# Kernel optimization log

Hardware: AMD Instinct MI355X
Metric: run time of the kernel (lower is better)

The kernel has to match this reference:

```python
import jax, jax.numpy as jnp
import numpy as np
import math

EPS = 1e-6          # eps for safe cumprod / clamping
CHUNK = 4           # chunk_size w
SHARP = 1.0         # sharpening_factor
NOISE_STD = 1.0
N_HEADS = 4
ADIM = 512


def moving_sum(x, back, forward):
    """Windowed running sum over last axis: out[k] = sum_{j=k-back}^{k+forward} x[j].
    Equivalent to the conv1d trick in the original (all-ones filter)."""
    k = x.shape[-1]
    pad = [(0, 0)] * (x.ndim - 1) + [(back, forward)]
    c = jnp.cumsum(jnp.pad(x, pad), axis=-1)
    c0 = jnp.concatenate([jnp.zeros_like(c[..., :1]), c], axis=-1)
    w = back + forward
    return c0[..., w + 1: w + 1 + k] - c0[..., :k]


def setup_inputs() -> dict:
    rng = jax.random.key(0)
    ks = jax.random.split(rng, 12)
    B, qlen, klen, kdim, qdim, adim = 8, 256, 2048, 512, 512, ADIM
    s = 0.02
    return {
        "key_enc": jax.random.normal(ks[0], (B, klen, kdim), jnp.float32),
        "query":   jax.random.normal(ks[1], (B, qlen, qdim), jnp.float32),
        "noise":   jax.random.normal(ks[2], (B, qlen, klen), jnp.float32),
        # monotonic energy params
        "Wk_m": jax.random.normal(ks[3], (kdim, adim), jnp.float32) * s,
        "bk_m": jnp.zeros((adim,), jnp.float32),
        "Wq_m": jax.random.normal(ks[4], (qdim, adim), jnp.float32) * s,
        "bq_m": jnp.zeros((adim,), jnp.float32),
        "r":    jnp.array([-4.0], jnp.float32),
        # chunkwise energy params (multi-head)
        "Wk_c": jax.random.normal(ks[5], (kdim, adim), jnp.float32) * s,
        "bk_c": jnp.zeros((adim,), jnp.float32),
        "Wq_c": jax.random.normal(ks[6], (qdim, adim), jnp.float32) * s,
        "bq_c": jnp.zeros((adim,), jnp.float32),
    }


def _mocha_beta(key_enc, query, noise, Wk_m, bk_m, Wq_m, bq_m, r,
                Wk_c, bk_c, Wq_c, bq_c):
    B, klen, _ = key_enc.shape
    qlen = query.shape[1]
    H = N_HEADS
    dk = ADIM // H
    scale = math.sqrt(ADIM)

    # --- monotonic energy (single head): [B, qlen, klen]
    k_m = key_enc @ Wk_m + bk_m
    q_m = query @ Wq_m + bq_m
    e_mono = jnp.einsum('bqa,bka->bqk', q_m, k_m) / scale + r[0]

    # --- p_choose with additive gaussian noise (encourages discreteness)
    p_choose = jax.nn.sigmoid(e_mono + noise * NOISE_STD)  # [B,q,k]

    # --- safe cumprod of (1 - p) via exclusive cumsum in log space
    log1mp = jnp.log(jnp.clip(1.0 - p_choose, EPS, 1.0))
    cumprod_1mp = jnp.exp(jnp.cumsum(log1mp, axis=-1) - log1mp)  # exclusive

    # --- monotonic alpha recurrence over query steps (parallel-mode MoChA)
    aw0 = jnp.zeros((B, klen), jnp.float32).at[:, 0].set(1.0)

    def step(aw_prev, inp):
        p_i, cp_i = inp  # [B, klen]
        alpha_i = p_i * cp_i * jnp.cumsum(
            aw_prev / jnp.clip(cp_i, EPS, 1.0), axis=-1)
        return alpha_i, alpha_i

    xs = (jnp.swapaxes(p_choose, 0, 1), jnp.swapaxes(cumprod_1mp, 0, 1))
    _, alpha_q = jax.lax.scan(step, aw0, xs)          # [q, B, k]
    alpha = jnp.swapaxes(alpha_q, 0, 1)                # [B, q, k]

    # --- chunkwise energy (multi-head): [B, H, q, k]
    k_c = (key_enc @ Wk_c + bk_c).reshape(B, klen, H, dk)
    q_c = (query @ Wq_c + bq_c).reshape(B, qlen, H, dk)
    e_chunk = jnp.einsum('bqhd,bkhd->bhqk', q_c, k_c) / scale

    # --- efficient chunkwise attention (clipped-logit moving-sum softmax)
    e = e_chunk - jnp.max(e_chunk, axis=3, keepdims=True)
    softmax_exp = jnp.maximum(jnp.exp(e), 1e-5)
    denom = moving_sum(softmax_exp, back=CHUNK - 1, forward=0)
    beta = softmax_exp * moving_sum(
        alpha[:, None] * SHARP / denom, back=0, forward=CHUNK - 1)
    return beta  # [B, H, q, k]


def reference(key_enc, query, noise, Wk_m, bk_m, Wq_m, bq_m, r,
              Wk_c, bk_c, Wq_c, bq_c):
    return _mocha_beta(key_enc, query, noise, Wk_m, bk_m, Wq_m, bq_m, r,
                       Wk_c, bk_c, Wq_c, bq_c)
```

## Files before the change

### kernel.cpp

```cpp
#include <hip/hip_runtime.h>
#include <math.h>

#define BATCH   8
#define QLEN    256
#define KLEN    2048
#define KDIM    512
#define ADIMC   512
#define NHEADS  4
#define DKH     128
#define CHUNKW  4

static constexpr float INV_SCALE = 0.04419417382415922f;
static constexpr float EPSV = 1e-6f;

typedef __attribute__((ext_vector_type(8))) short bf16x8;
typedef __attribute__((ext_vector_type(4))) float f32x4;

__device__ __forceinline__ unsigned short f2bf(float f) {
    unsigned u = __builtin_bit_cast(unsigned, f);
    u += 0x7fffu + ((u >> 16) & 1u);
    return (unsigned short)(u >> 16);
}

__device__ __forceinline__ void lds_barrier() {
    __asm__ volatile("s_waitcnt lgkmcnt(0)\n\ts_barrier" ::: "memory");
}

__device__ __forceinline__ void gload_lds16(const void* g, void* l) {
    __builtin_amdgcn_global_load_lds(
        (const __attribute__((address_space(1))) void*)g,
        (__attribute__((address_space(3))) void*)l, 16, 0, 0);
}

__global__ __launch_bounds__(256) void cast_bf16(
    const float* __restrict__ x, unsigned short* __restrict__ y, int n4)
{
    int i = blockIdx.x * 256 + threadIdx.x;
    if (i < n4) {
        float4 v = ((const float4*)x)[i];
        ushort4 o;
        o.x = f2bf(v.x); o.y = f2bf(v.y); o.z = f2bf(v.z); o.w = f2bf(v.w);
        ((ushort4*)y)[i] = o;
    }
}

__global__ __launch_bounds__(256) void transpose_cast(
    const float* __restrict__ W, unsigned short* __restrict__ WT)
{
    __shared__ float tile[32][33];
    const int tx = threadIdx.x;
    const int ty = threadIdx.y;
    const int k0 = blockIdx.y * 32, n0 = blockIdx.x * 32;
    #pragma unroll
    for (int i = 0; i < 32; i += 8)
        tile[ty + i][tx] = W[(size_t)(k0 + ty + i) * KDIM + n0 + tx];
    __syncthreads();
    #pragma unroll
    for (int i = 0; i < 32; i += 8)
        WT[(size_t)(n0 + ty + i) * KDIM + k0 + tx] = f2bf(tile[tx][ty + i]);
}

template<int KSTEPS>
__device__ __forceinline__ void mfma_nt_staged(
    const unsigned short* __restrict__ A, const unsigned short* __restrict__ B,
    int lda, int ldb, int bm, int bn,
    unsigned short* AsLDS, unsigned short* BsLDS, f32x4 acc[4][4])
{
    const int t = threadIdx.x;
    const int wv = t >> 6, ln = t & 63;
    const int r = ln & 15, quad = ln >> 4;
    const int wm = (wv >> 1) * 64, wn = (wv & 1) * 64;
    const int srow = wv * 16 + (ln >> 2);
    const int scol = (ln & 3) * 8;

    for (int ks = 0; ks < KSTEPS; ++ks) {
        const int k0 = ks * 32;
        #pragma unroll
        for (int j = 0; j < 2; ++j) {
            gload_lds16(A + (size_t)(bm + j * 64 + srow) * lda + k0 + scol,
                        AsLDS + (size_t)(j * 64 + wv * 16) * 32);
            gload_lds16(B + (size_t)(bn + j * 64 + srow) * ldb + k0 + scol,
                        BsLDS + (size_t)(j * 64 + wv * 16) * 32);
        }
        __syncthreads();
        bf16x8 af[4], bg[4];
        #pragma unroll
        for (int f = 0; f < 4; ++f)
            af[f] = *(const bf16x8*)(AsLDS + (size_t)(wm + f * 16 + r) * 32 + quad * 8);
        #pragma unroll
        for (int f = 0; f < 4; ++f)
            bg[f] = *(const bf16x8*)(BsLDS + (size_t)(wn + f * 16 + r) * 32 + quad * 8);
        #pragma unroll
        for (int i = 0; i < 4; ++i)
            #pragma unroll
            for (int j2 = 0; j2 < 4; ++j2)
                acc[i][j2] = __builtin_amdgcn_mfma_f32_16x16x32_bf16(
                    af[i], bg[j2], acc[i][j2], 0, 0, 0);
        __syncthreads();
    }
}

__device__ __forceinline__ void zero_acc(f32x4 acc[4][4]) {
    #pragma unroll
    for (int i = 0; i < 4; ++i)
        #pragma unroll
        for (int j = 0; j < 4; ++j)
            acc[i][j] = f32x4{0.f, 0.f, 0.f, 0.f};
}

__global__ __launch_bounds__(256) void proj_mfma(
    const unsigned short* __restrict__ A, const unsigned short* __restrict__ WT,
    const float* __restrict__ bias_m, const float* __restrict__ bias_c,
    unsigned short* __restrict__ C)
{
    __shared__ unsigned short As[128 * 32];
    __shared__ unsigned short Bs[128 * 32];
    const int bm = blockIdx.y * 128, bn = blockIdx.x * 128;
    f32x4 acc[4][4]; zero_acc(acc);
    mfma_nt_staged<16>(A, WT, KDIM, KDIM, bm, bn, As, Bs, acc);
    const int wv = threadIdx.x >> 6, ln = threadIdx.x & 63;
    const int r = ln & 15, quad = ln >> 4;
    const int m0 = bm + (wv >> 1) * 64, n0 = bn + (wv & 1) * 64;
    #pragma unroll
    for (int j = 0; j < 4; ++j) {
        const int n = n0 + j * 16 + r;
        const float bv = (n < 512) ? bias_m[n] : bias_c[n - 512];
        #pragma unroll
        for (int i = 0; i < 4; ++i) {
            #pragma unroll
            for (int reg = 0; reg < 4; ++reg) {
                const int m = m0 + i * 16 + quad * 4 + reg;
                C[(size_t)m * 1024 + n] = f2bf(acc[i][j][reg] + bv);
            }
        }
    }
}

__global__ __launch_bounds__(256) void pchoose_mfma(
    const unsigned short* __restrict__ qp, const unsigned short* __restrict__ kp,
    const float* __restrict__ noise, const float* __restrict__ rp,
    float* __restrict__ p)
{
    __shared__ unsigned short As[128 * 32];
    __shared__ unsigned short Bs[128 * 32];
    const int b = blockIdx.z;
    const unsigned short* A = qp + (size_t)b * QLEN * 1024;
    const unsigned short* B = kp + (size_t)b * KLEN * 1024;
    const int bm = blockIdx.y * 128, bn = blockIdx.x * 128;
    f32x4 acc[4][4]; zero_acc(acc);
    mfma_nt_staged<16>(A, B, 1024, 1024, bm, bn, As, Bs, acc);
    const int wv = threadIdx.x >> 6, ln = threadIdx.x & 63;
    const int r = ln & 15, quad = ln >> 4;
    const int m0 = bm + (wv >> 1) * 64, n0 = bn + (wv & 1) * 64;
    const float rv = rp[0];
    #pragma unroll
    for (int i = 0; i < 4; ++i) {
        #pragma unroll
        for (int reg = 0; reg < 4; ++reg) {
            const int q = m0 + i * 16 + quad * 4 + reg;
            const size_t rowoff = ((size_t)b * QLEN + q) * KLEN;
            #pragma unroll
            for (int j = 0; j < 4; ++j) {
                const int k = n0 + j * 16 + r;
                const float e = acc[i][j][reg] * INV_SCALE + rv + noise[rowoff + k];
                p[rowoff + k] = __builtin_amdgcn_rcpf(1.0f + __expf(-e));
            }
        }
    }
}

__global__ __launch_bounds__(256) void echunk_mfma(
    const unsigned short* __restrict__ qp, const unsigned short* __restrict__ kp,
    float* __restrict__ out)
{
    __shared__ unsigned short As[128 * 32];
    __shared__ unsigned short Bs[128 * 32];
    const int z = blockIdx.z, b = z >> 2, h = z & 3;
    const unsigned short* A = qp + (size_t)b * QLEN * 1024 + 512 + h * DKH;
    const unsigned short* B = kp + (size_t)b * KLEN * 1024 + 512 + h * DKH;
    const int bm = blockIdx.y * 128, bn = blockIdx.x * 128;
    f32x4 acc[4][4]; zero_acc(acc);
    mfma_nt_staged<4>(A, B, 1024, 1024, bm, bn, As, Bs, acc);
    const int wv = threadIdx.x >> 6, ln = threadIdx.x & 63;
    const int r = ln & 15, quad = ln >> 4;
    const int m0 = bm + (wv >> 1) * 64, n0 = bn + (wv & 1) * 64;
    #pragma unroll
    for (int i = 0; i < 4; ++i) {
        #pragma unroll
        for (int reg = 0; reg < 4; ++reg) {
            const int q = m0 + i * 16 + quad * 4 + reg;
            const size_t rowoff = (((size_t)z) * QLEN + q) * KLEN;
            #pragma unroll
            for (int j = 0; j < 4; ++j) {
                const int k = n0 + j * 16 + r;
                out[rowoff + k] = acc[i][j][reg] * INV_SCALE;
            }
        }
    }
}

__device__ __forceinline__ float wave_incl_scan(float x)
{
#define DPP_ADD(ctrl, rmask, bctrl)                                            \
    { int _t = __builtin_amdgcn_update_dpp(0, __builtin_bit_cast(int, x),      \
                                           ctrl, rmask, 0xf, bctrl);           \
      x += __builtin_bit_cast(float, _t); }
    DPP_ADD(0x111, 0xf, true)
    DPP_ADD(0x112, 0xf, true)
    DPP_ADD(0x114, 0xf, true)
    DPP_ADD(0x118, 0xf, true)
    DPP_ADD(0x142, 0xa, false)
    DPP_ADD(0x143, 0xc, false)
#undef DPP_ADD
    return x;
}

__global__ __launch_bounds__(256) void cumprod_mr(
    const float* __restrict__ p, float* __restrict__ mArr, float* __restrict__ rArr)
{
    const size_t row = blockIdx.x;
    const float* pr = p + row * KLEN;
    float* mr = mArr + row * KLEN;
    float* rr = rArr + row * KLEN;
    const int tid = threadIdx.x;
    const int lane = tid & 63, wid = tid >> 6;
    __shared__ float waveTot[4];

    float4 v0 = *(const float4*)(pr + tid * 8);
    float4 v1 = *(const float4*)(pr + tid * 8 + 4);
    float pv[8] = {v0.x, v0.y, v0.z, v0.w, v1.x, v1.y, v1.z, v1.w};
    float excl[8];
    float run = 0.0f;
    #pragma unroll
    for (int j = 0; j < 8; ++j) {
        float l = __logf(fminf(fmaxf(1.0f - pv[j], EPSV), 1.0f));
        excl[j] = run;
        run += l;
    }
    float s = wave_incl_scan(run);
    if (lane == 63) waveTot[wid] = s;
    __syncthreads();
    float wex = 0.0f;
    for (int w = 0; w < wid; ++w) wex += waveTot[w];
    const float texcl = wex + s - run;

    float mv[8], rv[8];
    #pragma unroll
    for (int j = 0; j < 8; ++j) {
        const float cpv = __expf(texcl + excl[j]);
        mv[j] = pv[j] * cpv;
        rv[j] = __builtin_amdgcn_rcpf(fminf(fmaxf(cpv, EPSV), 1.0f));
    }
    *(float4*)(mr + tid * 8)     = *(float4*)&mv[0];
    *(float4*)(mr + tid * 8 + 4) = *(float4*)&mv[4];
    *(float4*)(rr + tid * 8)     = *(float4*)&rv[0];
    *(float4*)(rr + tid * 8 + 4) = *(float4*)&rv[4];
}

__global__ __launch_bounds__(512, 1) void alpha_scan(
    const float* __restrict__ mArr, const float* __restrict__ rArr,
    float* __restrict__ alpha)
{
    const int b = blockIdx.x;
    const int tid = threadIdx.x;
    const int lane = tid & 63, wid = tid >> 6;
    __shared__ __align__(16) float wt[2][8];

    const float* mrow = mArr + (size_t)b * QLEN * KLEN + tid * 4;
    const float* rrow = rArr + (size_t)b * QLEN * KLEN + tid * 4;
    float* arow = alpha + (size_t)b * QLEN * KLEN + tid * 4;

    float aw0 = 0.f, aw1 = 0.f, aw2 = 0.f, aw3 = 0.f;
    if (tid == 0) aw0 = 1.0f;

    float4 mA = *(const float4*)(mrow);
    float4 rA = *(const float4*)(rrow);
    float4 mB = *(const float4*)(mrow + KLEN);
    float4 rB = *(const float4*)(rrow + KLEN);

#define ASTEP(I, MREG, RREG)                                                   \
    {                                                                          \
        const int i_ = (I);                                                    \
        float4 mc = MREG, rc = RREG;                                           \
        const int rn_ = (i_ + 2 < QLEN) ? (i_ + 2) : (QLEN - 1);               \
        MREG = *(const float4*)(mrow + (size_t)rn_ * KLEN);                    \
        RREG = *(const float4*)(rrow + (size_t)rn_ * KLEN);                    \
        float run = 0.0f, i0, i1, i2, i3;                                      \
        run = fmaf(aw0, rc.x, run); i0 = run;                                  \
        run = fmaf(aw1, rc.y, run); i1 = run;                                  \
        run = fmaf(aw2, rc.z, run); i2 = run;                                  \
        run = fmaf(aw3, rc.w, run); i3 = run;                                  \
        float tot = wave_incl_scan(run);                                       \
        if (lane == 63) wt[i_ & 1][wid] = tot;                                 \
        lds_barrier();                                                         \
        float base = tot - run;                                                \
        float4 w0 = *(const float4*)&wt[i_ & 1][0];                            \
        float4 w1 = *(const float4*)&wt[i_ & 1][4];                            \
        if (wid > 0) base += w0.x;                                             \
        if (wid > 1) base += w0.y;                                             \
        if (wid > 2) base += w0.z;                                             \
        if (wid > 3) base += w0.w;                                             \
        if (wid > 4) base += w1.x;                                             \
        if (wid > 5) base += w1.y;                                             \
        if (wid > 6) base += w1.z;                                             \
        aw0 = mc.x * (base + i0);                                              \
        aw1 = mc.y * (base + i1);                                              \
        aw2 = mc.z * (base + i2);                                              \
        aw3 = mc.w * (base + i3);                                              \
        float4 ov; ov.x = aw0; ov.y = aw1; ov.z = aw2; ov.w = aw3;             \
        *(float4*)(arow + (size_t)i_ * KLEN) = ov;                             \
    }

    for (int io = 0; io < QLEN; io += 2) {
        ASTEP(io + 0, mA, rA)
        ASTEP(io + 1, mB, rB)
    }
#undef ASTEP
}

__global__ __launch_bounds__(256) void beta_kernel(
    float* __restrict__ eo, const float* __restrict__ alpha)
{
    __shared__ float sse[KLEN + 3];
    __shared__ float su[KLEN + 3];
    __shared__ float wmax[4];

    const int tid = threadIdx.x;
    const int lane = tid & 63, wid = tid >> 6;
    const int row = blockIdx.x;
    const int q = row & (QLEN - 1);
    const int b = row >> 10;
    float* erow = eo + (size_t)row * KLEN;
    const float* arow = alpha + ((size_t)b * QLEN + q) * KLEN;

    if (tid < 3) { sse[tid] = 0.0f; su[KLEN + tid] = 0.0f; }

    float ev[8];
    float lm = -INFINITY;
    #pragma unroll
    for (int j = 0; j < 8; ++j) {
        const int k = tid + 256 * j;
        ev[j] = erow[k];
        lm = fmaxf(lm, ev[j]);
    }
    #pragma unroll
    for (int off = 32; off > 0; off >>= 1) lm = fmaxf(lm, __shfl_xor(lm, off));
    if (lane == 0) wmax[wid] = lm;
    __syncthreads();
    const float mx = fmaxf(fmaxf(wmax[0], wmax[1]), fmaxf(wmax[2], wmax[3]));

    #pragma unroll
    for (int j = 0; j < 8; ++j) {
        const int k = tid + 256 * j;
        sse[k + 3] = fmaxf(__expf(ev[j] - mx), 1e-5f);
    }
    __syncthreads();

    #pragma unroll
    for (int j = 0; j < 8; ++j) {
        const int k = tid + 256 * j;
        const float denom = sse[k + 3] + sse[k + 2] + sse[k + 1] + sse[k];
        su[k] = arow[k] * __builtin_amdgcn_rcpf(denom);
    }
    __syncthreads();

    #pragma unroll
    for (int j = 0; j < 8; ++j) {
        const int k = tid + 256 * j;
        erow[k] = sse[k + 3] * (su[k] + su[k + 1] + su[k + 2] + su[k + 3]);
    }
}

extern "C" void kernel_launch(void* const* d_in, const int* in_sizes, int n_in,
                              void* d_out, int out_size, void* d_ws, size_t ws_size,
                              hipStream_t stream)
{
    (void)in_sizes; (void)n_in; (void)out_size; (void)ws_size;
    const float* key_enc = (const float*)d_in[0];
    const float* query   = (const float*)d_in[1];
    const float* noise   = (const float*)d_in[2];
    const float* Wk_m    = (const float*)d_in[3];
    const float* bk_m    = (const float*)d_in[4];
    const float* Wq_m    = (const float*)d_in[5];
    const float* bq_m    = (const float*)d_in[6];
    const float* rp      = (const float*)d_in[7];
    const float* Wk_c    = (const float*)d_in[8];
    const float* bk_c    = (const float*)d_in[9];
    const float* Wq_c    = (const float*)d_in[10];
    const float* bq_c    = (const float*)d_in[11];
    float* out = (float*)d_out;

    char* w = (char*)d_ws;
    unsigned short* kx    = (unsigned short*)w; w += (size_t)BATCH * KLEN * KDIM * 2;
    unsigned short* qx    = (unsigned short*)w; w += (size_t)BATCH * QLEN * KDIM * 2;
    unsigned short* WTk   = (unsigned short*)w; w += (size_t)1024 * KDIM * 2;
    unsigned short* WTq   = (unsigned short*)w; w += (size_t)1024 * KDIM * 2;
    unsigned short* kproj = (unsigned short*)w; w += (size_t)BATCH * KLEN * 1024 * 2;
    unsigned short* qproj = (unsigned short*)w; w += (size_t)BATCH * QLEN * 1024 * 2;
    float* p_alpha = (float*)w; w += (size_t)BATCH * QLEN * KLEN * 4;
    float* mArr    = (float*)w; w += (size_t)BATCH * QLEN * KLEN * 4;
    float* rArr    = (float*)w;

    hipLaunchKernelGGL(cast_bf16, dim3(BATCH * KLEN * KDIM / 4 / 256), dim3(256), 0, stream,
                       key_enc, kx, BATCH * KLEN * KDIM / 4);
    hipLaunchKernelGGL(cast_bf16, dim3(BATCH * QLEN * KDIM / 4 / 256), dim3(256), 0, stream,
                       query, qx, BATCH * QLEN * KDIM / 4);
    hipLaunchKernelGGL(transpose_cast, dim3(16, 16), dim3(32, 8), 0, stream, Wk_m, WTk);
    hipLaunchKernelGGL(transpose_cast, dim3(16, 16), dim3(32, 8), 0, stream, Wk_c, WTk + (size_t)512 * KDIM);
    hipLaunchKernelGGL(transpose_cast, dim3(16, 16), dim3(32, 8), 0, stream, Wq_m, WTq);
    hipLaunchKernelGGL(transpose_cast, dim3(16, 16), dim3(32, 8), 0, stream, Wq_c, WTq + (size_t)512 * KDIM);

    hipLaunchKernelGGL(proj_mfma, dim3(8, BATCH * KLEN / 128), dim3(256), 0, stream,
                       kx, WTk, bk_m, bk_c, kproj);
    hipLaunchKernelGGL(proj_mfma, dim3(8, BATCH * QLEN / 128), dim3(256), 0, stream,
                       qx, WTq, bq_m, bq_c, qproj);

    hipLaunchKernelGGL(pchoose_mfma, dim3(KLEN / 128, QLEN / 128, BATCH), dim3(256), 0, stream,
                       qproj, kproj, noise, rp, p_alpha);

    hipLaunchKernelGGL(cumprod_mr, dim3(BATCH * QLEN), dim3(256), 0, stream,
                       p_alpha, mArr, rArr);

    hipLaunchKernelGGL(alpha_scan, dim3(BATCH), dim3(512), 0, stream,
                       mArr, rArr, p_alpha);

    hipLaunchKernelGGL(echunk_mfma, dim3(KLEN / 128, QLEN / 128, BATCH * NHEADS), dim3(256), 0, stream,
                       qproj, kproj, out);

    hipLaunchKernelGGL(beta_kernel, dim3(BATCH * NHEADS * QLEN), dim3(256), 0, stream,
                       out, p_alpha);
}
```

Measured before the change: 323.9 us.

## Rewrite alpha scan as single-wave-per-batch to drop LDS barriers

The sequential alpha recurrence now runs one 64-lane wave per batch, each lane owning 32 contiguous elements, instead of 512 threads with 4 elements each. This removes the per-row cross-wave LDS exchange and s_barrier, leaving only an intra-wave scan. Prefetch depth goes from 2 to 3 rows ahead. The trade-offs are a longer serial FMA chain per lane, heavy register use, and only 8 wavefronts in total, which leaves per-row load latency and memory bandwidth for this serial kernel less hidden.

```diff
diff --git a/kernel.cpp b/kernel.cpp
--- a/kernel.cpp
+++ b/kernel.cpp
@@ -20,10 +20,6 @@
     unsigned u = __builtin_bit_cast(unsigned, f);
     u += 0x7fffu + ((u >> 16) & 1u);
     return (unsigned short)(u >> 16);
-}
-
-__device__ __forceinline__ void lds_barrier() {
-    __asm__ volatile("s_waitcnt lgkmcnt(0)\n\ts_barrier" ::: "memory");
 }
 
 __device__ __forceinline__ void gload_lds16(const void* g, void* l) {
@@ -257,65 +253,115 @@
     *(float4*)(rr + tid * 8 + 4) = *(float4*)&rv[4];
 }
 
-__global__ __launch_bounds__(512, 1) void alpha_scan(
+__global__ __launch_bounds__(64) void alpha_scan(
     const float* __restrict__ mArr, const float* __restrict__ rArr,
     float* __restrict__ alpha)
 {
     const int b = blockIdx.x;
-    const int tid = threadIdx.x;
-    const int lane = tid & 63, wid = tid >> 6;
-    __shared__ __align__(16) float wt[2][8];
-
-    const float* mrow = mArr + (size_t)b * QLEN * KLEN + tid * 4;
-    const float* rrow = rArr + (size_t)b * QLEN * KLEN + tid * 4;
-    float* arow = alpha + (size_t)b * QLEN * KLEN + tid * 4;
-
-    float aw0 = 0.f, aw1 = 0.f, aw2 = 0.f, aw3 = 0.f;
-    if (tid == 0) aw0 = 1.0f;
-
-    float4 mA = *(const float4*)(mrow);
-    float4 rA = *(const float4*)(rrow);
-    float4 mB = *(const float4*)(mrow + KLEN);
-    float4 rB = *(const float4*)(rrow + KLEN);
-
-#define ASTEP(I, MREG, RREG)                                                   \
+    const int t = threadIdx.x;
+    const float* mrow = mArr + (size_t)b * QLEN * KLEN + t * 32;
+    const float* rrow = rArr + (size_t)b * QLEN * KLEN + t * 32;
+    float* arow = alpha + (size_t)b * QLEN * KLEN + t * 32;
+
+    const float4 z4 = {0.f, 0.f, 0.f, 0.f};
+    float4 a0 = z4, a1 = z4, a2 = z4, a3 = z4, a4 = z4, a5 = z4, a6 = z4, a7 = z4;
+    if (t == 0) a0.x = 1.0f;
+
+#define LOADROW8(M0,M1,M2,M3,M4,M5,M6,M7, src)                                 \
+    M0 = *(const float4*)((src) + 0);  M1 = *(const float4*)((src) + 4);       \
+    M2 = *(const float4*)((src) + 8);  M3 = *(const float4*)((src) + 12);      \
+    M4 = *(const float4*)((src) + 16); M5 = *(const float4*)((src) + 20);      \
+    M6 = *(const float4*)((src) + 24); M7 = *(const float4*)((src) + 28);
+
+    float4 mA0,mA1,mA2,mA3,mA4,mA5,mA6,mA7, rA0,rA1,rA2,rA3,rA4,rA5,rA6,rA7;
+    float4 mB0,mB1,mB2,mB3,mB4,mB5,mB6,mB7, rB0,rB1,rB2,rB3,rB4,rB5,rB6,rB7;
+    float4 mC0,mC1,mC2,mC3,mC4,mC5,mC6,mC7, rC0,rC1,rC2,rC3,rC4,rC5,rC6,rC7;
+    LOADROW8(mA0,mA1,mA2,mA3,mA4,mA5,mA6,mA7, mrow)
+    LOADROW8(rA0,rA1,rA2,rA3,rA4,rA5,rA6,rA7, rrow)
+    LOADROW8(mB0,mB1,mB2,mB3,mB4,mB5,mB6,mB7, mrow + KLEN)
+    LOADROW8(rB0,rB1,rB2,rB3,rB4,rB5,rB6,rB7, rrow + KLEN)
+    LOADROW8(mC0,mC1,mC2,mC3,mC4,mC5,mC6,mC7, mrow + 2 * KLEN)
+    LOADROW8(rC0,rC1,rC2,rC3,rC4,rC5,rC6,rC7, rrow + 2 * KLEN)
+
+#define ASTEP(I, M0,M1,M2,M3,M4,M5,M6,M7, R0,R1,R2,R3,R4,R5,R6,R7)             \
     {                                                                          \
         const int i_ = (I);                                                    \
-        float4 mc = MREG, rc = RREG;                                           \
-        const int rn_ = (i_ + 2 < QLEN) ? (i_ + 2) : (QLEN - 1);               \
-        MREG = *(const float4*)(mrow + (size_t)rn_ * KLEN);                    \
-        RREG = *(const float4*)(rrow + (size_t)rn_ * KLEN);                    \
-        float run = 0.0f, i0, i1, i2, i3;                                      \
-        run = fmaf(aw0, rc.x, run); i0 = run;                                  \
-        run = fmaf(aw1, rc.y, run); i1 = run;                                  \
-        run = fmaf(aw2, rc.z, run); i2 = run;                                  \
-        run = fmaf(aw3, rc.w, run); i3 = run;                                  \
-        float tot = wave_incl_scan(run);                                       \
-        if (lane == 63) wt[i_ & 1][wid] = tot;                                 \
-        lds_barrier();                                                         \
-        float base = tot - run;                                                \
-        float4 w0 = *(const float4*)&wt[i_ & 1][0];                            \
-        float4 w1 = *(const float4*)&wt[i_ & 1][4];                            \
-        if (wid > 0) base += w0.x;                                             \
-        if (wid > 1) base += w0.y;                                             \
-        if (wid > 2) base += w0.z;                                             \
-        if (wid > 3) base += w0.w;                                             \
-        if (wid > 4) base += w1.x;                                             \
-        if (wid > 5) base += w1.y;                                             \
-        if (wid > 6) base += w1.z;                                             \
-        aw0 = mc.x * (base + i0);                                              \
-        aw1 = mc.y * (base + i1);                                              \
-        aw2 = mc.z * (base + i2);                                              \
-        aw3 = mc.w * (base + i3);                                              \
-        float4 ov; ov.x = aw0; ov.y = aw1; ov.z = aw2; ov.w = aw3;             \
-        *(float4*)(arow + (size_t)i_ * KLEN) = ov;                             \
-    }
-
-    for (int io = 0; io < QLEN; io += 2) {
-        ASTEP(io + 0, mA, rA)
-        ASTEP(io + 1, mB, rB)
-    }
+                                  \
+        float run0 = 0.0f;                                                     \
+        run0 = fmaf(a0.x, R0.x, run0); const float i00 = run0;                 \
+        run0 = fmaf(a0.y, R0.y, run0); const float i01 = run0;                 \
+        run0 = fmaf(a0.z, R0.z, run0); const float i02 = run0;                 \
+        run0 = fmaf(a0.w, R0.w, run0); const float i03 = run0;                 \
+        run0 = fmaf(a1.x, R1.x, run0); const float i10 = run0;                 \
+        run0 = fmaf(a1.y, R1.y, run0); const float i11 = run0;                 \
+        run0 = fmaf(a1.z, R1.z, run0); const float i12 = run0;                 \
+        run0 = fmaf(a1.w, R1.w, run0); const float i13 = run0;                 \
+        run0 = fmaf(a2.x, R2.x, run0); const float i20 = run0;                 \
+        run0 = fmaf(a2.y, R2.y, run0); const float i21 = run0;                 \
+        run0 = fmaf(a2.z, R2.z, run0); const float i22 = run0;                 \
+        run0 = fmaf(a2.w, R2.w, run0); const float i23 = run0;                 \
+        run0 = fmaf(a3.x, R3.x, run0); const float i30 = run0;                 \
+        run0 = fmaf(a3.y, R3.y, run0); const float i31 = run0;                 \
+        run0 = fmaf(a3.z, R3.z, run0); const float i32 = run0;                 \
+        run0 = fmaf(a3.w, R3.w, run0); const float i33 = run0;                 \
+        float run1 = 0.0f;                                                     \
+        run1 = fmaf(a4.x, R4.x, run1); const float i40 = run1;                 \
+        run1 = fmaf(a4.y, R4.y, run1); const float i41 = run1;                 \
+        run1 = fmaf(a4.z, R4.z, run1); const float i42 = run1;                 \
+        run1 = fmaf(a4.w, R4.w, run1); const float i43 = run1;                 \
+        run1 = fmaf(a5.x, R5.x, run1); const float i50 = run1;                 \
+        run1 = fmaf(a5.y, R5.y, run1); const float i51 = run1;                 \
+        run1 = fmaf(a5.z, R5.z, run1); const float i52 = run1;                 \
+        run1 = fmaf(a5.w, R5.w, run1); const float i53 = run1;                 \
+        run1 = fmaf(a6.x, R6.x, run1); const float i60 = run1;                 \
+        run1 = fmaf(a6.y, R6.y, run1); const float i61 = run1;                 \
+        run1 = fmaf(a6.z, R6.z, run1); const float i62 = run1;                 \
+        run1 = fmaf(a6.w, R6.w, run1); const float i63 = run1;                 \
+        run1 = fmaf(a7.x, R7.x, run1); const float i70 = run1;                 \
+        run1 = fmaf(a7.y, R7.y, run1); const float i71 = run1;                 \
+        run1 = fmaf(a7.z, R7.z, run1); const float i72 = run1;                 \
+        run1 = fmaf(a7.w, R7.w, run1); const float i73 = run1;                 \
+        const float tin = run0 + run1;                                         \
+        const float tot = wave_incl_scan(tin);                                 \
+        const float base = tot - tin;                \
+        const float bhi = base + run0;                                         \
+        a0.x = M0.x * (base + i00); a0.y = M0.y * (base + i01);                \
+        a0.z = M0.z * (base + i02); a0.w = M0.w * (base + i03);                \
+        a1.x = M1.x * (base + i10); a1.y = M1.y * (base + i11);                \
+        a1.z = M1.z * (base + i12); a1.w = M1.w * (base + i13);                \
+        a2.x = M2.x * (base + i20); a2.y = M2.y * (base + i21);                \
+        a2.z = M2.z * (base + i22); a2.w = M2.w * (base + i23);                \
+        a3.x = M3.x * (base + i30); a3.y = M3.y * (base + i31);                \
+        a3.z = M3.z * (base + i32); a3.w = M3.w * (base + i33);                \
+        a4.x = M4.x * (bhi + i40);  a4.y = M4.y * (bhi + i41);                 \
+        a4.z = M4.z * (bhi + i42);  a4.w = M4.w * (bhi + i43);                 \
+        a5.x = M5.x * (bhi + i50);  a5.y = M5.y * (bhi + i51);                 \
+        a5.z = M5.z * (bhi + i52);  a5.w = M5.w * (bhi + i53);                 \
+        a6.x = M6.x * (bhi + i60);  a6.y = M6.y * (bhi + i61);                 \
+        a6.z = M6.z * (bhi + i62);  a6.w = M6.w * (bhi + i63);                 \
+        a7.x = M7.x * (bhi + i70);  a7.y = M7.y * (bhi + i71);                 \
+        a7.z = M7.z * (bhi + i72);  a7.w = M7.w * (bhi + i73);                 \
+        float* o_ = arow + (size_t)i_ * KLEN;                                  \
+        *(float4*)(o_ + 0)  = a0; *(float4*)(o_ + 4)  = a1;                    \
+        *(float4*)(o_ + 8)  = a2; *(float4*)(o_ + 12) = a3;                    \
+        *(float4*)(o_ + 16) = a4; *(float4*)(o_ + 20) = a5;                    \
+        *(float4*)(o_ + 24) = a6; *(float4*)(o_ + 28) = a7;                    \
+                       \
+        const int rn_ = (i_ + 3 < QLEN) ? (i_ + 3) : (QLEN - 1);               \
+        const float* mp_ = mrow + (size_t)rn_ * KLEN;                          \
+        const float* rq_ = rrow + (size_t)rn_ * KLEN;                          \
+        LOADROW8(M0,M1,M2,M3,M4,M5,M6,M7, mp_)                                 \
+        LOADROW8(R0,R1,R2,R3,R4,R5,R6,R7, rq_)                                 \
+    }
+
+    for (int io = 0; io < 255; io += 3) {
+        ASTEP(io + 0, mA0,mA1,mA2,mA3,mA4,mA5,mA6,mA7, rA0,rA1,rA2,rA3,rA4,rA5,rA6,rA7)
+        ASTEP(io + 1, mB0,mB1,mB2,mB3,mB4,mB5,mB6,mB7, rB0,rB1,rB2,rB3,rB4,rB5,rB6,rB7)
+        ASTEP(io + 2, mC0,mC1,mC2,mC3,mC4,mC5,mC6,mC7, rC0,rC1,rC2,rC3,rC4,rC5,rC6,rC7)
+    }
+    ASTEP(255, mA0,mA1,mA2,mA3,mA4,mA5,mA6,mA7, rA0,rA1,rA2,rA3,rA4,rA5,rA6,rA7)
 #undef ASTEP
+#undef LOADROW8
 }
 
 __global__ __launch_bounds__(256) void beta_kernel(
@@ -421,7 +467,7 @@
     hipLaunchKernelGGL(cumprod_mr, dim3(BATCH * QLEN), dim3(256), 0, stream,
                        p_alpha, mArr, rArr);
 
-    hipLaunchKernelGGL(alpha_scan, dim3(BATCH), dim3(512), 0, stream,
+    hipLaunchKernelGGL(alpha_scan, dim3(BATCH), dim3(64), 0, stream,
                        mArr, rArr, p_alpha);
 
     hipLaunchKernelGGL(echunk_mfma, dim3(KLEN / 128, QLEN / 128, BATCH * NHEADS), dim3(256), 0, stream,
```

New measurement: 564.5 us. +74.3%, slower.

## Fuse alpha scan and chunk-energy GEMM into one heterogeneous launch

Applied to the files above, without the earlier changes.

Merges the serial alpha_scan kernel (8 blocks) and the echunk MFMA GEMM into one launch. The first 8 blocks run the per-batch scan and the remaining blocks compute the chunkwise energy tiles with 256 of their 512 threads. The aim is to fill the GPU while the latency-bound scan runs, instead of running the two back to back. The cost is that GEMM blocks now use 512-thread blocks with half the threads idle and an unpipelined staging loop, which may lower GEMM efficiency and occupancy.

```diff
diff --git a/kernel.cpp b/kernel.cpp
--- a/kernel.cpp
+++ b/kernel.cpp
@@ -169,36 +169,6 @@
     }
 }
 
-__global__ __launch_bounds__(256) void echunk_mfma(
-    const unsigned short* __restrict__ qp, const unsigned short* __restrict__ kp,
-    float* __restrict__ out)
-{
-    __shared__ unsigned short As[128 * 32];
-    __shared__ unsigned short Bs[128 * 32];
-    const int z = blockIdx.z, b = z >> 2, h = z & 3;
-    const unsigned short* A = qp + (size_t)b * QLEN * 1024 + 512 + h * DKH;
-    const unsigned short* B = kp + (size_t)b * KLEN * 1024 + 512 + h * DKH;
-    const int bm = blockIdx.y * 128, bn = blockIdx.x * 128;
-    f32x4 acc[4][4]; zero_acc(acc);
-    mfma_nt_staged<4>(A, B, 1024, 1024, bm, bn, As, Bs, acc);
-    const int wv = threadIdx.x >> 6, ln = threadIdx.x & 63;
-    const int r = ln & 15, quad = ln >> 4;
-    const int m0 = bm + (wv >> 1) * 64, n0 = bn + (wv & 1) * 64;
-    #pragma unroll
-    for (int i = 0; i < 4; ++i) {
-        #pragma unroll
-        for (int reg = 0; reg < 4; ++reg) {
-            const int q = m0 + i * 16 + quad * 4 + reg;
-            const size_t rowoff = (((size_t)z) * QLEN + q) * KLEN;
-            #pragma unroll
-            for (int j = 0; j < 4; ++j) {
-                const int k = n0 + j * 16 + r;
-                out[rowoff + k] = acc[i][j][reg] * INV_SCALE;
-            }
-        }
-    }
-}
-
 __device__ __forceinline__ float wave_incl_scan(float x)
 {
 #define DPP_ADD(ctrl, rmask, bctrl)                                            \
@@ -257,26 +227,30 @@
     *(float4*)(rr + tid * 8 + 4) = *(float4*)&rv[4];
 }
 
-__global__ __launch_bounds__(512, 1) void alpha_scan(
+__global__ __launch_bounds__(512, 1) void alpha_echunk(
     const float* __restrict__ mArr, const float* __restrict__ rArr,
-    float* __restrict__ alpha)
-{
-    const int b = blockIdx.x;
+    float* __restrict__ alpha,
+    const unsigned short* __restrict__ qp, const unsigned short* __restrict__ kp,
+    float* __restrict__ out)
+{
+    __shared__ __align__(16) char smem[16384];
+    const int bid = blockIdx.x;
     const int tid = threadIdx.x;
-    const int lane = tid & 63, wid = tid >> 6;
-    __shared__ __align__(16) float wt[2][8];
-
-    const float* mrow = mArr + (size_t)b * QLEN * KLEN + tid * 4;
-    const float* rrow = rArr + (size_t)b * QLEN * KLEN + tid * 4;
-    float* arow = alpha + (size_t)b * QLEN * KLEN + tid * 4;
-
-    float aw0 = 0.f, aw1 = 0.f, aw2 = 0.f, aw3 = 0.f;
-    if (tid == 0) aw0 = 1.0f;
-
-    float4 mA = *(const float4*)(mrow);
-    float4 rA = *(const float4*)(rrow);
-    float4 mB = *(const float4*)(mrow + KLEN);
-    float4 rB = *(const float4*)(rrow + KLEN);
+
+    if (bid < BATCH) {
+        float (*wt)[8] = (float (*)[8])smem;
+        const int lane = tid & 63, wid = tid >> 6;
+        const float* mrow = mArr + (size_t)bid * QLEN * KLEN + tid * 4;
+        const float* rrow = rArr + (size_t)bid * QLEN * KLEN + tid * 4;
+        float* arow = alpha + (size_t)bid * QLEN * KLEN + tid * 4;
+
+        float aw0 = 0.f, aw1 = 0.f, aw2 = 0.f, aw3 = 0.f;
+        if (tid == 0) aw0 = 1.0f;
+
+        float4 mA = *(const float4*)(mrow);
+        float4 rA = *(const float4*)(rrow);
+        float4 mB = *(const float4*)(mrow + KLEN);
+        float4 rB = *(const float4*)(rrow + KLEN);
 
 #define ASTEP(I, MREG, RREG)                                                   \
     {                                                                          \
@@ -311,11 +285,78 @@
         *(float4*)(arow + (size_t)i_ * KLEN) = ov;                             \
     }
 
-    for (int io = 0; io < QLEN; io += 2) {
-        ASTEP(io + 0, mA, rA)
-        ASTEP(io + 1, mB, rB)
-    }
+        for (int io = 0; io < QLEN; io += 2) {
+            ASTEP(io + 0, mA, rA)
+            ASTEP(io + 1, mB, rB)
+        }
 #undef ASTEP
+        return;
+    }
+
+    const int v = bid - BATCH;
+    const int z = v >> 5;
+    const int by = (v >> 4) & 1;
+    const int bx = v & 15;
+    const int b = z >> 2, h = z & 3;
+    const bool worker = tid < 256;
+    unsigned short* As = (unsigned short*)smem;
+    unsigned short* Bs = (unsigned short*)(smem + 8192);
+    const unsigned short* A = qp + (size_t)b * QLEN * 1024 + 512 + h * DKH;
+    const unsigned short* B = kp + (size_t)b * KLEN * 1024 + 512 + h * DKH;
+    const int bm = by * 128, bn = bx * 128;
+
+    const int wv = tid >> 6, ln = tid & 63;
+    const int r = ln & 15, quad = ln >> 4;
+    const int wm = (wv >> 1) * 64, wn = (wv & 1) * 64;
+    const int srow = (wv & 3) * 16 + (ln >> 2);
+    const int scol = (ln & 3) * 8;
+
+    f32x4 acc[4][4]; zero_acc(acc);
+    for (int ks = 0; ks < 4; ++ks) {
+        const int k0 = ks * 32;
+        if (worker) {
+            #pragma unroll
+            for (int j = 0; j < 2; ++j) {
+                gload_lds16(A + (size_t)(bm + j * 64 + srow) * 1024 + k0 + scol,
+                            As + (size_t)(j * 64 + wv * 16) * 32);
+                gload_lds16(B + (size_t)(bn + j * 64 + srow) * 1024 + k0 + scol,
+                            Bs + (size_t)(j * 64 + wv * 16) * 32);
+            }
+        }
+        __syncthreads();
+        if (worker) {
+            bf16x8 af[4], bg[4];
+            #pragma unroll
+            for (int f = 0; f < 4; ++f)
+                af[f] = *(const bf16x8*)(As + (size_t)(wm + f * 16 + r) * 32 + quad * 8);
+            #pragma unroll
+            for (int f = 0; f < 4; ++f)
+                bg[f] = *(const bf16x8*)(Bs + (size_t)(wn + f * 16 + r) * 32 + quad * 8);
+            #pragma unroll
+            for (int i = 0; i < 4; ++i)
+                #pragma unroll
+                for (int j2 = 0; j2 < 4; ++j2)
+                    acc[i][j2] = __builtin_amdgcn_mfma_f32_16x16x32_bf16(
+                        af[i], bg[j2], acc[i][j2], 0, 0, 0);
+        }
+        __syncthreads();
+    }
+    if (worker) {
+        const int m0 = bm + (wv >> 1) * 64, n0 = bn + (wv & 1) * 64;
+        #pragma unroll
+        for (int i = 0; i < 4; ++i) {
+            #pragma unroll
+            for (int reg = 0; reg < 4; ++reg) {
+                const int q = m0 + i * 16 + quad * 4 + reg;
+                const size_t rowoff = ((size_t)z * QLEN + q) * KLEN;
+                #pragma unroll
+                for (int j = 0; j < 4; ++j) {
+                    const int k = n0 + j * 16 + r;
+                    out[rowoff + k] = acc[i][j][reg] * INV_SCALE;
+                }
+            }
+        }
+    }
 }
 
 __global__ __launch_bounds__(256) void beta_kernel(
@@ -421,11 +462,9 @@
     hipLaunchKernelGGL(cumprod_mr, dim3(BATCH * QLEN), dim3(256), 0, stream,
                        p_alpha, mArr, rArr);
 
-    hipLaunchKernelGGL(alpha_scan, dim3(BATCH), dim3(512), 0, stream,
-                       mArr, rArr, p_alpha);
-
-    hipLaunchKernelGGL(echunk_mfma, dim3(KLEN / 128, QLEN / 128, BATCH * NHEADS), dim3(256), 0, stream,
-                       qproj, kproj, out);
+    hipLaunchKernelGGL(alpha_echunk, dim3(BATCH + KLEN / 128 * QLEN / 128 * BATCH * NHEADS),
+                       dim3(512), 0, stream,
+                       mArr, rArr, p_alpha, qproj, kproj, out);
 
     hipLaunchKernelGGL(beta_kernel, dim3(BATCH * NHEADS * QLEN), dim3(256), 0, stream,
                        out, p_alpha);
```

Result: faster. 311.5 us (-3.8%).
